# Optimization experiments

Measured on AMD Instinct MI355X. Metric: run time of the kernel, lower is better.

Reference implementation:

```python
import jax, jax.numpy as jnp
import numpy as np

N = 128      # n_ab: number of independent tiny MLPs
H = 128      # hidden width
L = 4097     # odd alpha grid length, alpha[L//2] == pi/2


def setup_inputs() -> dict:
    key = jax.random.key(0)
    ks = jax.random.split(key, 10)
    alpha = jnp.linspace(0.0, np.pi, L).astype(jnp.float32)
    s = 1.0 / np.sqrt(H)
    w0 = jax.random.normal(ks[0], (N, H, 1), dtype=jnp.float32) * 0.5
    w1 = jax.random.normal(ks[1], (N, H, H), dtype=jnp.float32) * s
    w2 = jax.random.normal(ks[2], (N, H, H), dtype=jnp.float32) * s
    w3 = jax.random.normal(ks[3], (N, 1, H), dtype=jnp.float32) * s
    b0 = jax.random.normal(ks[4], (N, H), dtype=jnp.float32) * 0.1
    b1 = jax.random.normal(ks[5], (N, H), dtype=jnp.float32) * 0.1
    b2 = jax.random.normal(ks[6], (N, H), dtype=jnp.float32) * 0.1
    b3 = jax.random.normal(ks[7], (N, 1), dtype=jnp.float32) * 0.1 + 1.0
    sqrt_a = jax.random.uniform(ks[8], (N,), dtype=jnp.float32, minval=0.5, maxval=1.5)
    return dict(alpha=alpha, w0=w0, w1=w1, w2=w2, w3=w3,
                b0=b0, b1=b1, b2=b2, b3=b3, sqrt_a=sqrt_a)


def _mlp_b(alpha_half, ws, bs):
    # alpha_half: (B,) -> b: (N, B)
    n = ws[0].shape[0]
    x = jnp.broadcast_to(alpha_half[None, :, None], (n, alpha_half.shape[0], 1))
    for w, b in zip(ws[:-1], bs[:-1]):
        x = jax.nn.relu(jnp.einsum('Nij,NBj->NBi', w, x) + b[:, None, :])
    x = jnp.einsum('Nij,NBj->NBi', ws[-1], x) + bs[-1][:, None, :]
    return jnp.square(x)[..., 0]  # (N, B)


def reference(alpha, w0, w1, w2, w3, b0, b1, b2, b3, sqrt_a):
    half = alpha[: alpha.shape[0] // 2 + 1]  # first half incl. pi/2
    ws, bs = (w0, w1, w2, w3), (b0, b1, b2, b3)
    # db/dalpha via jvp with unit tangent: each b[n, j] depends only on
    # alpha_half[j], matching the torch double-autograd trick through z.
    b, db = jax.jvp(lambda a: _mlp_b(a, ws, bs), (half,), (jnp.ones_like(half),))
    b_full = jnp.concatenate([b, b[:, :-1][:, ::-1]], axis=1)          # (N, L)
    db_full = jnp.concatenate([db, -db[:, :-1][:, ::-1]], axis=1)      # (N, L)
    a_full = jnp.square(sqrt_a)[:, None]                               # (N, 1)
    al = alpha[None, :]                                                # (1, L)
    xp = a_full * (jnp.cos(al) - 1.0)
    yp = b_full * jnp.sin(al)
    xp_prime = jnp.broadcast_to(-a_full * jnp.sin(al), b_full.shape)
    yp_prime = b_full * jnp.cos(al) + db_full * jnp.sin(al)
    return xp, yp, xp_prime, yp_prime
```

## Files before the change

### kernel.cpp

```cpp
#include <hip/hip_runtime.h>
#include <math.h>

#define NN 128
#define HH 128
#define LL 4097
#define PH 2049
#define BP2 32
#define NT2 65
#define BP 64
#define NTILE 33
#define WS_NEEDED (2u * 128u * 64u * 64u * 16u)

typedef short bf16x8 __attribute__((ext_vector_type(8)));
typedef float f32x4  __attribute__((ext_vector_type(4)));
typedef unsigned int u32;

__device__ __forceinline__ void split1(float x, u32& hi, u32& lo) {
    u32 bx = __float_as_uint(x);
    hi = bx >> 16;
    float hf = __uint_as_float(bx & 0xffff0000u);
    float d  = x - hf;
    lo = (__float_as_uint(d) + 0x8000u) >> 16;
}

__device__ __forceinline__ f32x4 MF(bf16x8 a, bf16x8 b, f32x4 c) {
    return __builtin_amdgcn_mfma_f32_16x16x32_bf16(a, b, c, 0, 0, 0);
}


__global__ __launch_bounds__(512) void presplit(
    const float* __restrict__ w1, const float* __restrict__ w2, uint4* __restrict__ ws)
{
    const int b = blockIdx.x;
    const int m = b >> 7, n = b & 127;
    const float* wn = (m ? w2 : w1) + n * HH * HH;
    uint4* dst = ws + b * 4096;
    const int tid = threadIdx.x;
#pragma unroll
    for (int it = 0; it < 4; ++it) {
        const int s  = tid + it * 512;
        const int l  = s & 63;
        const int fq = s >> 6;
        const int ks = fq & 3, it7 = fq >> 2;
        const int i  = it7 * 16 + (l & 15);
        const int k0 = ks * 32 + (l >> 4) * 8;
        const float4* src = (const float4*)(wn + i * HH + k0);
        const float4 va = src[0], vb = src[1];
        const float v[8] = {va.x, va.y, va.z, va.w, vb.x, vb.y, vb.z, vb.w};
        u32 hd[4], ld_[4];
#pragma unroll
        for (int q = 0; q < 4; ++q) {
            u32 h0, l0, h1, l1;
            split1(v[2*q], h0, l0); split1(v[2*q+1], h1, l1);
            hd[q]  = h0 | (h1 << 16);
            ld_[q] = l0 | (l1 << 16);
        }
        dst[(fq*2 + 0)*64 + l] = make_uint4(hd[0], hd[1], hd[2], hd[3]);
        dst[(fq*2 + 1)*64 + l] = make_uint4(ld_[0], ld_[1], ld_[2], ld_[3]);
    }
}

__device__ __forceinline__ void gemm_regW(const bf16x8* __restrict__ Wf, const char* Xb,
                                          f32x4 acc[4][2], int rw, int cw, int l) {
    const bf16x8* Xf = (const bf16x8*)Xb;
#pragma unroll
    for (int ks = 0; ks < 4; ++ks) {
        bf16x8 Bh[2], Bl[2];
#pragma unroll
        for (int cg = 0; cg < 2; ++cg) {
            const int ct = cw + cg * 2;
            Bh[cg] = Xf[((ct*4 + ks)*2 + 0)*64 + l];
            Bl[cg] = Xf[((ct*4 + ks)*2 + 1)*64 + l];
        }
#pragma unroll
        for (int itl = 0; itl < 4; ++itl) {
            const int IT = rw * 4 + itl;
            const bf16x8 Ah = Wf[((IT*4 + ks)*2 + 0)*64 + l];
            const bf16x8 Al = Wf[((IT*4 + ks)*2 + 1)*64 + l];
#pragma unroll
            for (int cg = 0; cg < 2; ++cg) {
                acc[itl][cg] = MF(Ah, Bh[cg], acc[itl][cg]);
                acc[itl][cg] = MF(Ah, Bl[cg], acc[itl][cg]);
                acc[itl][cg] = MF(Al, Bh[cg], acc[itl][cg]);
            }
        }
    }
}

__global__ __launch_bounds__(256, 5) void sofa_mfma3(
    const float* __restrict__ alpha,
    const float* __restrict__ w0, const float* __restrict__ w3,
    const float* __restrict__ b0, const float* __restrict__ b1,
    const float* __restrict__ b2, const float* __restrict__ b3,
    const float* __restrict__ sqrt_a,
    const uint4* __restrict__ ws,
    float* __restrict__ out)
{
    __shared__ char smem[32768];
    char*  Xb  = smem;
    float* red = (float*)smem;

    const int tile = blockIdx.x, n = blockIdx.y;
    const int tid = threadIdx.x;
    const int l   = tid & 63;
    const int w   = tid >> 6;
    const int rw  = __builtin_amdgcn_readfirstlane(w & 1);
    const int cw  = __builtin_amdgcn_readfirstlane(w >> 1);
    const int t   = l >> 4;

    const bf16x8* W1f = (const bf16x8*)(ws + n * 4096);
    const bf16x8* W2f = (const bf16x8*)(ws + (128 + n) * 4096);

    {
        const float* w0n = w0 + n * HH;
        const float* b0n = b0 + n * HH;
        const int c  = tid & 63;
        const int jb = tid >> 6;
        int p = tile * BP2 + (c & 31);
        if (p > 2048) p = 2048;
        const float a = alpha[p];
        const bool isdh = c >= 32;
        const int ct = c >> 4;
#pragma unroll
        for (int g8 = 0; g8 < 4; ++g8) {
            const float4 wv4a = *(const float4*)(w0n + jb*32 + g8*8);
            const float4 wv4b = *(const float4*)(w0n + jb*32 + g8*8 + 4);
            const float4 bv4a = *(const float4*)(b0n + jb*32 + g8*8);
            const float4 bv4b = *(const float4*)(b0n + jb*32 + g8*8 + 4);
            const float wvv[8] = {wv4a.x,wv4a.y,wv4a.z,wv4a.w,wv4b.x,wv4b.y,wv4b.z,wv4b.w};
            const float bvv[8] = {bv4a.x,bv4a.y,bv4a.z,bv4a.w,bv4b.x,bv4b.y,bv4b.z,bv4b.w};
            u32 hd[4], ld_[4];
#pragma unroll
            for (int q = 0; q < 4; ++q) {
                float vv[2];
#pragma unroll
                for (int e = 0; e < 2; ++e) {
                    const float wv  = wvv[q*2 + e];
                    const float pre = fmaf(wv, a, bvv[q*2 + e]);
                    const bool  on  = pre > 0.f;
                    vv[e] = isdh ? (on ? wv : 0.f) : (on ? pre : 0.f);
                }
                u32 h0, l0, h1, l1;
                split1(vv[0], h0, l0); split1(vv[1], h1, l1);
                hd[q]  = h0 | (h1 << 16);
                ld_[q] = l0 | (l1 << 16);
            }
            const int lane = g8 * 16 + (c & 15);
            const int fq   = ct * 4 + jb;
            *(uint4*)(Xb + ((fq*2 + 0)*64 + lane)*16) = make_uint4(hd[0], hd[1], hd[2], hd[3]);
            *(uint4*)(Xb + ((fq*2 + 1)*64 + lane)*16) = make_uint4(ld_[0], ld_[1], ld_[2], ld_[3]);
        }
    }
    __syncthreads();

    f32x4 acc[4][2];
#pragma unroll
    for (int i0 = 0; i0 < 4; ++i0)
#pragma unroll
        for (int c0 = 0; c0 < 2; ++c0) { f32x4 z = {0.f,0.f,0.f,0.f}; acc[i0][c0] = z; }
    __builtin_amdgcn_s_setprio(1);
    gemm_regW(W1f, Xb, acc, rw, cw, l);
    __builtin_amdgcn_s_setprio(0);

    u32 px[4][2][2][2];
    {
        const float* b1n = b1 + n * HH;
#pragma unroll
        for (int itl = 0; itl < 4; ++itl) {
            const int ibase = (rw*4 + itl)*16 + t*4;
            float hv[4], dv[4];
#pragma unroll
            for (int r = 0; r < 4; ++r) {
                const float pre = acc[itl][0][r] + b1n[ibase + r];
                const bool  on  = pre > 0.f;
                hv[r] = on ? pre : 0.f;
                dv[r] = on ? acc[itl][1][r] : 0.f;
            }
#pragma unroll
            for (int cg = 0; cg < 2; ++cg) {
                const float* vs = cg ? dv : hv;
                u32 a0,c0,a1,c1,a2,c2,a3,c3;
                split1(vs[0],a0,c0); split1(vs[1],a1,c1);
                split1(vs[2],a2,c2); split1(vs[3],a3,c3);
                px[itl][cg][0][0] = a0 | (a1 << 16);
                px[itl][cg][0][1] = a2 | (a3 << 16);
                px[itl][cg][1][0] = c0 | (c1 << 16);
                px[itl][cg][1][1] = c2 | (c3 << 16);
            }
        }
    }
    __syncthreads();

    {
#pragma unroll
        for (int itl = 0; itl < 4; ++itl) {
            const int IT   = rw*4 + itl;
            const int lane = ((IT & 1)*2 + (t >> 1))*16 + (l & 15);
            const int off8 = (t & 1)*8;
            const int ksn  = IT >> 1;
#pragma unroll
            for (int cg = 0; cg < 2; ++cg) {
                const int fq = (cw + cg*2)*4 + ksn;
#pragma unroll
                for (int hl = 0; hl < 2; ++hl) {
                    uint2 vv; vv.x = px[itl][cg][hl][0]; vv.y = px[itl][cg][hl][1];
                    *(uint2*)(Xb + ((fq*2 + hl)*64 + lane)*16 + off8) = vv;
                }
            }
        }
    }
    __syncthreads();

    f32x4 acc2[4][2];
#pragma unroll
    for (int i0 = 0; i0 < 4; ++i0)
#pragma unroll
        for (int c0 = 0; c0 < 2; ++c0) { f32x4 z = {0.f,0.f,0.f,0.f}; acc2[i0][c0] = z; }
    __builtin_amdgcn_s_setprio(1);
    gemm_regW(W2f, Xb, acc2, rw, cw, l);
    __builtin_amdgcn_s_setprio(0);

    float sh = 0.f, sd = 0.f;
    {
        const float* b2n = b2 + n * HH;
        const float* w3n = w3 + n * HH;
#pragma unroll
        for (int itl = 0; itl < 4; ++itl) {
            const int ibase = (rw*4 + itl)*16 + t*4;
#pragma unroll
            for (int r = 0; r < 4; ++r) {
                const int   i   = ibase + r;
                const float pre = acc2[itl][0][r] + b2n[i];
                const bool  on  = pre > 0.f;
                const float hv  = on ? pre : 0.f;
                const float dv  = on ? acc2[itl][1][r] : 0.f;
                const float wv  = w3n[i];
                sh = fmaf(wv, hv, sh);
                sd = fmaf(wv, dv, sd);
            }
        }
    }
    sh += __shfl_xor(sh, 16); sh += __shfl_xor(sh, 32);
    sd += __shfl_xor(sd, 16); sd += __shfl_xor(sd, 32);
    __syncthreads();
    if (t == 0) {
        const int col = cw * 16 + (l & 15);
        red[rw * 32 + col]       = sh;
        red[64 + rw * 32 + col]  = sd;
    }
    __syncthreads();

    if (tid < 32) {
        const float oo = b3[n] + red[tid] + red[32 + tid];
        const float d2 = red[64 + tid] + red[96 + tid];
        const float bb = oo * oo;
        const float db = 2.f * oo * d2;
        const float sa = sqrt_a[n];
        const float af = sa * sa;
        const int   NL = NN * LL;
        const int   k1 = tile * BP2 + tid;
        if (k1 < PH) {
            const float al = alpha[k1];
            const float sn = __sinf(al), cs = __cosf(al);
            const int base = n * LL + k1;
            out[base]          = af * (cs - 1.f);
            out[NL + base]     = bb * sn;
            out[2 * NL + base] = -af * sn;
            out[3 * NL + base] = fmaf(bb, cs, db * sn);
            if (k1 <= PH - 2) {
                const int base2 = n * LL + (LL - 1) - k1;
                out[base2]          = af * (-cs - 1.f);
                out[NL + base2]     = bb * sn;
                out[2 * NL + base2] = -af * sn;
                out[3 * NL + base2] = fmaf(bb, -cs, -db * sn);
            }
        }
    }
}


__device__ __forceinline__ void stageW_fb(const float* __restrict__ wn, char* Wb, int tid) {
#pragma unroll
    for (int it = 0; it < 4; ++it) {
        const int s  = tid + it * 512;
        const int l  = s & 63;
        const int fq = s >> 6;
        const int ks = fq & 3, it7 = fq >> 2;
        const int i  = it7 * 16 + (l & 15);
        const int k0 = ks * 32 + (l >> 4) * 8;
        const float4* src = (const float4*)(wn + i * HH + k0);
        const float4 va = src[0], vb = src[1];
        const float v[8] = {va.x, va.y, va.z, va.w, vb.x, vb.y, vb.z, vb.w};
        u32 hd[4], ld_[4];
#pragma unroll
        for (int q = 0; q < 4; ++q) {
            u32 h0, l0, h1, l1;
            split1(v[2*q], h0, l0); split1(v[2*q+1], h1, l1);
            hd[q]  = h0 | (h1 << 16);
            ld_[q] = l0 | (l1 << 16);
        }
        *(uint4*)(Wb + (((fq*2)+0)*64 + l)*16) = make_uint4(hd[0], hd[1], hd[2], hd[3]);
        *(uint4*)(Wb + (((fq*2)+1)*64 + l)*16) = make_uint4(ld_[0], ld_[1], ld_[2], ld_[3]);
    }
}

__device__ __forceinline__ void gemm128_fb(const char* Wb, const char* Xb,
                                           f32x4 acc[4][2], int rw, int cw, int l) {
    const bf16x8* Wf = (const bf16x8*)Wb;
    const bf16x8* Xf = (const bf16x8*)Xb;
#pragma unroll
    for (int ks = 0; ks < 4; ++ks) {
        bf16x8 Bh[2], Bl[2];
#pragma unroll
        for (int cg = 0; cg < 2; ++cg) {
            const int ct = cw + cg * 4;
            Bh[cg] = Xf[((ct*4 + ks)*2 + 0)*64 + l];
            Bl[cg] = Xf[((ct*4 + ks)*2 + 1)*64 + l];
        }
#pragma unroll
        for (int itl = 0; itl < 4; ++itl) {
            const int IT = rw * 4 + itl;
            const bf16x8 Ah = Wf[((IT*4 + ks)*2 + 0)*64 + l];
            const bf16x8 Al = Wf[((IT*4 + ks)*2 + 1)*64 + l];
#pragma unroll
            for (int cg = 0; cg < 2; ++cg) {
                acc[itl][cg] = MF(Ah, Bh[cg], acc[itl][cg]);
                acc[itl][cg] = MF(Ah, Bl[cg], acc[itl][cg]);
                acc[itl][cg] = MF(Al, Bh[cg], acc[itl][cg]);
            }
        }
    }
}

__global__ __launch_bounds__(512, 2) void sofa_mfma_fb(
    const float* __restrict__ alpha,
    const float* __restrict__ w0, const float* __restrict__ w1,
    const float* __restrict__ w2, const float* __restrict__ w3,
    const float* __restrict__ b0, const float* __restrict__ b1,
    const float* __restrict__ b2, const float* __restrict__ b3,
    const float* __restrict__ sqrt_a,
    float* __restrict__ out)
{
    __shared__ char smem[131072];
    char* Wb = smem;
    char* Xb = smem + 65536;
    float* red = (float*)smem;

    const int tile = blockIdx.x, n = blockIdx.y;
    const int tid = threadIdx.x;
    const int l   = tid & 63;
    const int w   = tid >> 6;
    const int rw  = w & 1;
    const int cw  = w >> 1;
    const int t   = l >> 4;

    stageW_fb(w1 + n * HH * HH, Wb, tid);
    {
        const float* w0n = w0 + n * HH;
        const float* b0n = b0 + n * HH;
        const int c  = tid & 127;
        const int jb = tid >> 7;
        int p = tile * BP + (c & 63);
        if (p > 2048) p = 2048;
        const float a = alpha[p];
        const bool isdh = c >= 64;
        const int ct = c >> 4;
#pragma unroll
        for (int g8 = 0; g8 < 4; ++g8) {
            u32 hd[4], ld_[4];
#pragma unroll
            for (int q = 0; q < 4; ++q) {
                float vv[2];
#pragma unroll
                for (int e = 0; e < 2; ++e) {
                    const int j = jb * 32 + g8 * 8 + q * 2 + e;
                    const float wv  = w0n[j];
                    const float pre = fmaf(wv, a, b0n[j]);
                    const bool  on  = pre > 0.f;
                    vv[e] = isdh ? (on ? wv : 0.f) : (on ? pre : 0.f);
                }
                u32 h0, l0, h1, l1;
                split1(vv[0], h0, l0); split1(vv[1], h1, l1);
                hd[q]  = h0 | (h1 << 16);
                ld_[q] = l0 | (l1 << 16);
            }
            const int lane = g8 * 16 + (c & 15);
            const int fq   = ct * 4 + jb;
            *(uint4*)(Xb + ((fq*2 + 0)*64 + lane)*16) = make_uint4(hd[0], hd[1], hd[2], hd[3]);
            *(uint4*)(Xb + ((fq*2 + 1)*64 + lane)*16) = make_uint4(ld_[0], ld_[1], ld_[2], ld_[3]);
        }
    }
    __syncthreads();

    f32x4 acc[4][2];
#pragma unroll
    for (int i0 = 0; i0 < 4; ++i0)
#pragma unroll
        for (int c0 = 0; c0 < 2; ++c0) { f32x4 z = {0.f,0.f,0.f,0.f}; acc[i0][c0] = z; }
    gemm128_fb(Wb, Xb, acc, rw, cw, l);

    u32 px[4][2][2][2];
    {
        const float* b1n = b1 + n * HH;
#pragma unroll
        for (int itl = 0; itl < 4; ++itl) {
            const int ibase = (rw*4 + itl)*16 + t*4;
            float hv[4], dv[4];
#pragma unroll
            for (int r = 0; r < 4; ++r) {
                const float pre = acc[itl][0][r] + b1n[ibase + r];
                const bool  on  = pre > 0.f;
                hv[r] = on ? pre : 0.f;
                dv[r] = on ? acc[itl][1][r] : 0.f;
            }
#pragma unroll
            for (int cg = 0; cg < 2; ++cg) {
                const float* vs = cg ? dv : hv;
                u32 a0,c0,a1,c1,a2,c2,a3,c3;
                split1(vs[0],a0,c0); split1(vs[1],a1,c1);
                split1(vs[2],a2,c2); split1(vs[3],a3,c3);
                px[itl][cg][0][0] = a0 | (a1 << 16);
                px[itl][cg][0][1] = a2 | (a3 << 16);
                px[itl][cg][1][0] = c0 | (c1 << 16);
                px[itl][cg][1][1] = c2 | (c3 << 16);
            }
        }
    }
    __syncthreads();

    stageW_fb(w2 + n * HH * HH, Wb, tid);
    {
#pragma unroll
        for (int itl = 0; itl < 4; ++itl) {
            const int IT   = rw*4 + itl;
            const int lane = ((IT & 1)*2 + (t >> 1))*16 + (l & 15);
            const int off8 = (t & 1)*8;
            const int ksn  = IT >> 1;
#pragma unroll
            for (int cg = 0; cg < 2; ++cg) {
                const int fq = (cw + cg*4)*4 + ksn;
#pragma unroll
                for (int hl = 0; hl < 2; ++hl) {
                    uint2 vv; vv.x = px[itl][cg][hl][0]; vv.y = px[itl][cg][hl][1];
                    *(uint2*)(Xb + ((fq*2 + hl)*64 + lane)*16 + off8) = vv;
                }
            }
        }
    }
    __syncthreads();

    f32x4 acc2[4][2];
#pragma unroll
    for (int i0 = 0; i0 < 4; ++i0)
#pragma unroll
        for (int c0 = 0; c0 < 2; ++c0) { f32x4 z = {0.f,0.f,0.f,0.f}; acc2[i0][c0] = z; }
    gemm128_fb(Wb, Xb, acc2, rw, cw, l);

    float sh = 0.f, sd = 0.f;
    {
        const float* b2n = b2 + n * HH;
        const float* w3n = w3 + n * HH;
#pragma unroll
        for (int itl = 0; itl < 4; ++itl) {
            const int ibase = (rw*4 + itl)*16 + t*4;
#pragma unroll
            for (int r = 0; r < 4; ++r) {
                const int   i   = ibase + r;
                const float pre = acc2[itl][0][r] + b2n[i];
                const bool  on  = pre > 0.f;
                const float hv  = on ? pre : 0.f;
                const float dv  = on ? acc2[itl][1][r] : 0.f;
                const float wv  = w3n[i];
                sh = fmaf(wv, hv, sh);
                sd = fmaf(wv, dv, sd);
            }
        }
    }
    sh += __shfl_xor(sh, 16); sh += __shfl_xor(sh, 32);
    sd += __shfl_xor(sd, 16); sd += __shfl_xor(sd, 32);
    __syncthreads();
    if (t == 0) {
        const int p = cw * 16 + (l & 15);
        red[rw * 64 + p]        = sh;
        red[128 + rw * 64 + p]  = sd;
    }
    __syncthreads();

    if (tid < 64) {
        const float oo = b3[n] + red[tid] + red[64 + tid];
        const float d2 = red[128 + tid] + red[192 + tid];
        const float bb = oo * oo;
        const float db = 2.f * oo * d2;
        const float sa = sqrt_a[n];
        const float af = sa * sa;
        const int   NL = NN * LL;
        const int   k1 = tile * BP + tid;
        if (k1 < PH) {
            {
                const float al = alpha[k1];
                const float sn = sinf(al), cs = cosf(al);
                const int base = n * LL + k1;
                out[base]          = af * (cs - 1.f);
                out[NL + base]     = bb * sn;
                out[2 * NL + base] = -af * sn;
                out[3 * NL + base] = fmaf(bb, cs, db * sn);
            }
            if (k1 <= PH - 2) {
                const int   k2  = (LL - 1) - k1;
                const float al2 = alpha[k2];
                const float sn2 = sinf(al2), cs2 = cosf(al2);
                const int base2 = n * LL + k2;
                out[base2]          = af * (cs2 - 1.f);
                out[NL + base2]     = bb * sn2;
                out[2 * NL + base2] = -af * sn2;
                out[3 * NL + base2] = fmaf(bb, cs2, -db * sn2);
            }
        }
    }
}

extern "C" void kernel_launch(void* const* d_in, const int* in_sizes, int n_in,
                              void* d_out, int out_size, void* d_ws, size_t ws_size,
                              hipStream_t stream) {
    const float* alpha  = (const float*)d_in[0];
    const float* w0     = (const float*)d_in[1];
    const float* w1     = (const float*)d_in[2];
    const float* w2     = (const float*)d_in[3];
    const float* w3     = (const float*)d_in[4];
    const float* b0     = (const float*)d_in[5];
    const float* b1     = (const float*)d_in[6];
    const float* b2     = (const float*)d_in[7];
    const float* b3     = (const float*)d_in[8];
    const float* sqrt_a = (const float*)d_in[9];
    (void)in_sizes; (void)n_in; (void)out_size;

    if (ws_size >= (size_t)WS_NEEDED) {
        uint4* ws = (uint4*)d_ws;
        presplit<<<256, 512, 0, stream>>>(w1, w2, ws);
        dim3 grid(NT2, NN);
        sofa_mfma3<<<grid, 256, 0, stream>>>(alpha, w0, w3, b0, b1, b2, b3,
                                             sqrt_a, ws, (float*)d_out);
    } else {
        dim3 grid(NTILE, NN);
        sofa_mfma_fb<<<grid, 512, 0, stream>>>(alpha, w0, w1, w2, w3,
                                               b0, b1, b2, b3, sqrt_a,
                                               (float*)d_out);
    }
}
```

Before: 219.6 us.

## Prefetch W1/W2 fragments into registers ahead of each GEMM

Loads each warp's split-bf16 weight fragments for W1 into a 32-entry register array before the layer-0 setup, and loads W2 fragments right after the first GEMM so they arrive during the ReLU/restaging phase. The goal is to hide global-memory latency that was previously exposed inside the MFMA loop. The cost is 128 extra VGPRs live across phases, which under launch_bounds(256,5) may force spills or limit occupancy.

```diff
diff --git a/kernel.cpp b/kernel.cpp
--- a/kernel.cpp
+++ b/kernel.cpp
@@ -60,8 +60,19 @@
     }
 }
 
-__device__ __forceinline__ void gemm_regW(const bf16x8* __restrict__ Wf, const char* Xb,
-                                          f32x4 acc[4][2], int rw, int cw, int l) {
+__device__ __forceinline__ void loadW(const bf16x8* __restrict__ Wf, bf16x8 Wreg[32],
+                                      int rw, int l) {
+#pragma unroll
+    for (int itl = 0; itl < 4; ++itl)
+#pragma unroll
+        for (int ks = 0; ks < 4; ++ks)
+#pragma unroll
+            for (int hl = 0; hl < 2; ++hl)
+                Wreg[(itl*4 + ks)*2 + hl] = Wf[(((rw*4 + itl)*4 + ks)*2 + hl)*64 + l];
+}
+
+__device__ __forceinline__ void gemm_Wreg(const bf16x8 Wreg[32], const char* Xb,
+                                          f32x4 acc[4][2], int cw, int l) {
     const bf16x8* Xf = (const bf16x8*)Xb;
 #pragma unroll
     for (int ks = 0; ks < 4; ++ks) {
@@ -74,9 +85,8 @@
         }
 #pragma unroll
         for (int itl = 0; itl < 4; ++itl) {
-            const int IT = rw * 4 + itl;
-            const bf16x8 Ah = Wf[((IT*4 + ks)*2 + 0)*64 + l];
-            const bf16x8 Al = Wf[((IT*4 + ks)*2 + 1)*64 + l];
+            const bf16x8 Ah = Wreg[(itl*4 + ks)*2 + 0];
+            const bf16x8 Al = Wreg[(itl*4 + ks)*2 + 1];
 #pragma unroll
             for (int cg = 0; cg < 2; ++cg) {
                 acc[itl][cg] = MF(Ah, Bh[cg], acc[itl][cg]);
@@ -87,7 +97,7 @@
     }
 }
 
-__global__ __launch_bounds__(256, 5) void sofa_mfma3(
+__global__ __launch_bounds__(256, 5) void sofa_mfma4(
     const float* __restrict__ alpha,
     const float* __restrict__ w0, const float* __restrict__ w3,
     const float* __restrict__ b0, const float* __restrict__ b1,
@@ -111,6 +121,9 @@
     const bf16x8* W1f = (const bf16x8*)(ws + n * 4096);
     const bf16x8* W2f = (const bf16x8*)(ws + (128 + n) * 4096);
 
+    bf16x8 Wreg[32];
+    loadW(W1f, Wreg, rw, l);
+
     {
         const float* w0n = w0 + n * HH;
         const float* b0n = b0 + n * HH;
@@ -159,8 +172,10 @@
 #pragma unroll
         for (int c0 = 0; c0 < 2; ++c0) { f32x4 z = {0.f,0.f,0.f,0.f}; acc[i0][c0] = z; }
     __builtin_amdgcn_s_setprio(1);
-    gemm_regW(W1f, Xb, acc, rw, cw, l);
+    gemm_Wreg(Wreg, Xb, acc, cw, l);
     __builtin_amdgcn_s_setprio(0);
+
+    loadW(W2f, Wreg, rw, l);
 
     u32 px[4][2][2][2];
     {
@@ -217,7 +232,7 @@
 #pragma unroll
         for (int c0 = 0; c0 < 2; ++c0) { f32x4 z = {0.f,0.f,0.f,0.f}; acc2[i0][c0] = z; }
     __builtin_amdgcn_s_setprio(1);
-    gemm_regW(W2f, Xb, acc2, rw, cw, l);
+    gemm_Wreg(Wreg, Xb, acc2, cw, l);
     __builtin_amdgcn_s_setprio(0);
 
     float sh = 0.f, sd = 0.f;
@@ -538,7 +553,7 @@
         uint4* ws = (uint4*)d_ws;
         presplit<<<256, 512, 0, stream>>>(w1, w2, ws);
         dim3 grid(NT2, NN);
-        sofa_mfma3<<<grid, 256, 0, stream>>>(alpha, w0, w3, b0, b1, b2, b3,
+        sofa_mfma4<<<grid, 256, 0, stream>>>(alpha, w0, w3, b0, b1, b2, b3,
                                              sqrt_a, ws, (float*)d_out);
     } else {
         dim3 grid(NTILE, NN);
```

Measured after the change: 536.8 us. +144.5%, slower.
